# Kernel tuning notes

Hardware: AMD Instinct MI355X
Metric: run time of the kernel (lower is better)

## Reference

```python
import jax, jax.numpy as jnp
import numpy as np

NUM_HEADS = 16


def setup_inputs() -> dict:
    key = jax.random.key(0)
    ks = jax.random.split(key, 5)
    N, L, E = 4, 1024, 1024
    x = jax.random.normal(ks[0], (N, L, E), dtype=jnp.float32)
    sc = 1.0 / np.sqrt(E)
    wq = jax.random.normal(ks[1], (E, E), dtype=jnp.float32) * sc
    wk = jax.random.normal(ks[2], (E, E), dtype=jnp.float32) * sc
    wv = jax.random.normal(ks[3], (E, E), dtype=jnp.float32) * sc
    wo = jax.random.normal(ks[4], (E, E), dtype=jnp.float32) * sc
    return {"x": x, "wq": wq, "wk": wk, "wv": wv, "wo": wo}


def reference(x, wq, wk, wv, wo):
    N, L, E = x.shape
    H = NUM_HEADS
    d = E // H  # d_k = d_v = d_q
    # Linear layers: y = x @ W^T (torch Linear weight is (out, in))
    q = (x @ wq.T).reshape(N, H, L, d)  # NOTE: raw view, matches torch .view
    k = (x @ wk.T).reshape(N, H, L, d)
    v = (x @ wv.T).reshape(N, H, L, d)
    scores = jnp.einsum("nhld,nhmd->nhlm", q, k) / jnp.sqrt(jnp.float32(d))
    # causal mask (dropout is identity in eval / p=0)
    causal = jnp.tril(jnp.ones((L, L), dtype=bool))
    scores = jnp.where(causal, scores, jnp.float32(-jnp.inf))
    attn = jax.nn.softmax(scores, axis=-1)
    wei = jnp.einsum("nhlm,nhmd->nhld", attn, v).reshape(N, L, H * d)
    return wei @ wo.T
```

## Files before the change

### kernel.cpp

```cpp
#include <hip/hip_runtime.h>
#include <hip/hip_bf16.h>

using bf16 = __hip_bfloat16;
typedef __attribute__((ext_vector_type(8))) short bf16x8;
typedef __attribute__((ext_vector_type(4))) float f32x4;

#define MFMA16(a, b, c) __builtin_amdgcn_mfma_f32_16x16x32_bf16(a, b, c, 0, 0, 0)
#define SWZ(row, byteoff) ((byteoff) ^ (((row) & 7) << 4))

__device__ __forceinline__ unsigned short f2b(float f) {
  union { float f; unsigned int u; } c; c.f = f;
  unsigned int r = c.u + 0x7fffu + ((c.u >> 16) & 1u);
  return (unsigned short)(r >> 16);
}
__device__ __forceinline__ float b2f(short b) {
  union { unsigned int u; float f; } c;
  c.u = ((unsigned int)(unsigned short)b) << 16;
  return c.f;
}
__device__ __forceinline__ bf16x8 scale8(bf16x8 v, float s) {
  bf16x8 r;
#pragma unroll
  for (int j = 0; j < 8; ++j) r[j] = (short)f2b(b2f(v[j]) * s);
  return r;
}
__device__ __forceinline__ unsigned cvtpk(float a, float b) {
  unsigned r;
  asm("v_cvt_pk_bf16_f32 %0, %1, %2" : "=v"(r) : "v"(a), "v"(b));
  return r;
}

__device__ __forceinline__ void gload_lds16(const void* g, void* l) {
  __builtin_amdgcn_global_load_lds(
      (const __attribute__((address_space(1))) void*)g,
      (__attribute__((address_space(3))) void*)l, 16, 0, 0);
}

__device__ __forceinline__ void store_out(float* p, float v) { *p = v; }
__device__ __forceinline__ void store_out(bf16* p, float v) {
  *(unsigned short*)p = f2b(v);
}

__global__ __launch_bounds__(256) void cast_all(
    const float* __restrict__ x, const float* __restrict__ wq,
    const float* __restrict__ wk, const float* __restrict__ wv,
    const float* __restrict__ wo,
    unsigned short* __restrict__ xb, unsigned short* __restrict__ wqb,
    unsigned short* __restrict__ wkb, unsigned short* __restrict__ wvb,
    unsigned short* __restrict__ wob) {
  int i = blockIdx.x * 256 + threadIdx.x;
  const float* src;
  unsigned short* dst;
  int off;
  if (i < 1048576) {
    src = x; dst = xb; off = i;
  } else {
    int j = i - 1048576;
    int seg = j >> 18;
    off = j & 262143;
    src = (seg == 0) ? wq : (seg == 1) ? wk : (seg == 2) ? wv : wo;
    dst = (seg == 0) ? wqb : (seg == 1) ? wkb : (seg == 2) ? wvb : wob;
  }
  float4 v = reinterpret_cast<const float4*>(src)[off];
  ushort4 o;
  o.x = f2b(v.x); o.y = f2b(v.y); o.z = f2b(v.z); o.w = f2b(v.w);
  reinterpret_cast<ushort4*>(dst)[off] = o;
}

template <typename TOUT>
__device__ __forceinline__ void gemm_tile(const bf16* __restrict__ A,
                                          const bf16* __restrict__ Bt,
                                          TOUT* __restrict__ C, int N, int K,
                                          int bm, int bn) {
  __shared__ bf16 Asm[128 * 64];
  __shared__ bf16 Bsm[128 * 64];
  const int tid = threadIdx.x;
  const int lane = tid & 63;
  const int w = tid >> 6;
  const int wr = w >> 1, wc = w & 1;
  const int fr = lane & 15;
  const int fg = lane >> 4;
  f32x4 acc[4][4] = {};

  const int strow = w * 8 + (lane >> 3);
  const int stcb = (lane & 7) * 16;

  for (int kt = 0; kt < K; kt += 64) {
#pragma unroll
    for (int r = 0; r < 4; ++r) {
      const int row = r * 32 + strow;
      gload_lds16(
          (const char*)(A + (size_t)(bm + row) * K + kt) + SWZ(row, stcb),
          (char*)Asm + (r * 32 + w * 8) * 128);
      gload_lds16(
          (const char*)(Bt + (size_t)row * K + kt) + SWZ(row, stcb),
          (char*)Bsm + (r * 32 + w * 8) * 128);
    }
    __syncthreads();
    bf16x8 afr[4][2], bfr[4][2];
#pragma unroll
    for (int m = 0; m < 4; ++m) {
      const int row = wr * 64 + m * 16 + fr;
      const char* rp = (const char*)Asm + row * 128;
#pragma unroll
      for (int s = 0; s < 2; ++s)
        afr[m][s] = *(const bf16x8*)(rp + SWZ(row, s * 64 + fg * 16));
    }
#pragma unroll
    for (int n = 0; n < 4; ++n) {
      const int row = wc * 64 + n * 16 + fr;
      const char* rp = (const char*)Bsm + row * 128;
#pragma unroll
      for (int s = 0; s < 2; ++s)
        bfr[n][s] = *(const bf16x8*)(rp + SWZ(row, s * 64 + fg * 16));
    }
    __builtin_amdgcn_s_setprio(1);
#pragma unroll
    for (int m = 0; m < 4; ++m)
#pragma unroll
      for (int n = 0; n < 4; ++n) {
        acc[m][n] = MFMA16(afr[m][0], bfr[n][0], acc[m][n]);
        acc[m][n] = MFMA16(afr[m][1], bfr[n][1], acc[m][n]);
      }
    __builtin_amdgcn_s_setprio(0);
    __syncthreads();
  }
#pragma unroll
  for (int m = 0; m < 4; ++m) {
    const int row0 = bm + wr * 64 + m * 16 + (lane >> 4) * 4;
#pragma unroll
    for (int n = 0; n < 4; ++n) {
      const int col = bn + wc * 64 + n * 16 + fr;
#pragma unroll
      for (int r = 0; r < 4; ++r)
        store_out(&C[(size_t)(row0 + r) * N + col], acc[m][n][r]);
    }
  }
}

__global__ __launch_bounds__(256) void gemm_qkv(
    const bf16* __restrict__ A, const bf16* __restrict__ B3,
    bf16* __restrict__ Cq, bf16* __restrict__ Ck, bf16* __restrict__ Cv) {
  const int id = blockIdx.y * 32 + blockIdx.x;
  const int sw = (id & 7) * 96 + (id >> 3);
  const int bm = (sw & 31) * 128;
  const int bnG = (sw >> 5) * 128;
  bf16* C = (bnG < 1024) ? Cq : (bnG < 2048) ? Ck : Cv;
  gemm_tile<bf16>(A, B3 + (size_t)bnG * 1024, C, 1024, 1024, bm, bnG & 1023);
}

__global__ __launch_bounds__(256) void gemm_out(const bf16* __restrict__ A,
                                                const bf16* __restrict__ B,
                                                float* __restrict__ C) {
  const int id = blockIdx.y * 32 + blockIdx.x;
  const int sw = (id & 7) * 32 + (id >> 3);
  const int bm = (sw & 31) * 128;
  const int bn = (sw >> 5) * 128;
  gemm_tile<float>(A, B + (size_t)bn * 1024, C, 1024, 1024, bm, bn);
}

__global__ __launch_bounds__(256) void attn_fwd(
    const bf16* __restrict__ Q, const bf16* __restrict__ K,
    const bf16* __restrict__ V, bf16* __restrict__ O) {
  const int nh = blockIdx.x;
  const size_t base = (size_t)nh * 65536;
  const bf16* Qp = Q + base;
  const bf16* Kp = K + base;
  const bf16* Vp = V + base;
  bf16* Op = O + base;
  const int p = blockIdx.y;
  const int qiA = p, qiB = 15 - p;
  const int tid = threadIdx.x;
  const int lane = tid & 63;
  const int w = tid >> 6;
  const int fr = lane & 15;
  const int fg = lane >> 4;

  __shared__ bf16 Ksm[2][64 * 64];
  __shared__ bf16 Vts[2][64 * 64];

  const float QSC = 0.125f * 1.44269504089f;
  const float MS = 12.0f;
  const int rA0 = qiA * 64 + w * 16;
  const int rB0 = qiB * 64 + w * 16;
  bf16x8 qA[2], qB[2];
#pragma unroll
  for (int ks = 0; ks < 2; ++ks) {
    qA[ks] = scale8(
        *(const bf16x8*)&Qp[(size_t)(rA0 + fr) * 64 + ks * 32 + fg * 8], QSC);
    qB[ks] = scale8(
        *(const bf16x8*)&Qp[(size_t)(rB0 + fr) * 64 + ks * 32 + fg * 8], QSC);
  }

  float sA = 0.f, sB = 0.f;
  f32x4 oA[4], oB[4];
#pragma unroll
  for (int d = 0; d < 4; ++d) {
    oA[d] = (f32x4){0.f, 0.f, 0.f, 0.f};
    oB[d] = (f32x4){0.f, 0.f, 0.f, 0.f};
  }

  const int NKV = qiB + 1;
  const int qloc = w * 16 + fr;

  const int bkv = (tid & 15) * 4;
  const int bd = (tid >> 4) * 4;
  union VU { ushort4 v; unsigned short s[4]; };
  VU v4[4], nv4[4];

  const int krow = w * 16 + (lane >> 3);
  const int kcb = (lane & 7) * 16;

#define STAGE_K(kt, bi)                                                       \
  {                                                                           \
    _Pragma("unroll") for (int i = 0; i < 2; ++i) {                           \
      const int row = krow + i * 8;                                           \
      gload_lds16((const char*)Kp + ((size_t)((kt)*64 + row) * 128 +          \
                                     SWZ(row, kcb)),                          \
                  (char*)&Ksm[bi][0] + (w * 16 + i * 8) * 128);               \
    }                                                                         \
  }
#define LOAD_V(kt, r)                                                         \
  {                                                                           \
    _Pragma("unroll") for (int j = 0; j < 4; ++j) (r)[j].v =                  \
        *(const ushort4*)(Vp + (size_t)((kt)*64 + bkv + j) * 64 + bd);        \
  }
#define WRITE_V(bi, r)                                                        \
  {                                                                           \
    _Pragma("unroll") for (int i = 0; i < 4; ++i) {                           \
      VU o4;                                                                  \
      _Pragma("unroll") for (int j = 0; j < 4; ++j) o4.s[j] = (r)[j].s[i];    \
      const int row = bd + i;                                                 \
      *(ushort4*)((char*)&Vts[bi][0] + row * 128 + SWZ(row, bkv * 2)) = o4.v; \
    }                                                                         \
  }

  STAGE_K(0, 0);
  LOAD_V(0, v4);
  WRITE_V(0, v4);
  __syncthreads();

  union PU { bf16x8 v; unsigned u[4]; };
  union VF { bf16x8 v; unsigned long long q[2]; };

  for (int kt = 0; kt < NKV; ++kt) {
    const int b = kt & 1;
    const bool more = (kt + 1 < NKV);
    if (more) {
      STAGE_K(kt + 1, b ^ 1);
      LOAD_V(kt + 1, nv4);
    }
    const bool aAct = (kt <= qiA);

    bf16x8 kf[4][2];
#pragma unroll
    for (int c = 0; c < 4; ++c) {
      const int row = c * 16 + fr;
      const char* rp = (const char*)&Ksm[b][0] + row * 128;
      kf[c][0] = *(const bf16x8*)(rp + SWZ(row, fg * 16));
      kf[c][1] = *(const bf16x8*)(rp + SWZ(row, 64 + fg * 16));
    }
    VF vf[4][2];
#pragma unroll
    for (int d = 0; d < 4; ++d) {
      const int row = d * 16 + fr;
      const char* rp = (const char*)&Vts[b][0] + row * 128;
#pragma unroll
      for (int ks = 0; ks < 2; ++ks) {
        vf[d][ks].q[0] =
            *(const unsigned long long*)(rp + SWZ(row, ks * 64 + fg * 8));
        vf[d][ks].q[1] =
            *(const unsigned long long*)(rp + SWZ(row, ks * 64 + 32 + fg * 8));
      }
    }

    auto strip_sm = [&](const bf16x8 (&qf)[2], float& s, bool diag,
                        PU (&pa)[2]) {
      f32x4 sc[4];
      __builtin_amdgcn_s_setprio(1);
#pragma unroll
      for (int c = 0; c < 4; ++c) {
        f32x4 acc = (f32x4){0.f, 0.f, 0.f, 0.f};
        acc = MFMA16(kf[c][0], qf[0], acc);
        acc = MFMA16(kf[c][1], qf[1], acc);
        sc[c] = acc;
      }
      __builtin_amdgcn_s_setprio(0);
      float pv[4][4];
#pragma unroll
      for (int c = 0; c < 4; ++c)
#pragma unroll
        for (int r = 0; r < 4; ++r) {
          float sv = sc[c][r];
          if (diag) {
            const int kvloc = c * 16 + fg * 4 + r;
            sv = (kvloc <= qloc) ? sv : -INFINITY;
          }
          const float e = __builtin_amdgcn_exp2f(sv - MS);
          pv[c][r] = e;
          s += e;
        }
#pragma unroll
      for (int ks = 0; ks < 2; ++ks) {
        pa[ks].u[0] = cvtpk(pv[ks * 2][0], pv[ks * 2][1]);
        pa[ks].u[1] = cvtpk(pv[ks * 2][2], pv[ks * 2][3]);
        pa[ks].u[2] = cvtpk(pv[ks * 2 + 1][0], pv[ks * 2 + 1][1]);
        pa[ks].u[3] = cvtpk(pv[ks * 2 + 1][2], pv[ks * 2 + 1][3]);
      }
    };

    PU paA[2], paB[2];
    strip_sm(qB, sB, kt == qiB, paB);
    if (aAct) strip_sm(qA, sA, kt == qiA, paA);

    __builtin_amdgcn_s_setprio(1);
#pragma unroll
    for (int d = 0; d < 4; ++d) {
      oB[d] = MFMA16(paB[0].v, vf[d][0].v, oB[d]);
      oB[d] = MFMA16(paB[1].v, vf[d][1].v, oB[d]);
    }
    if (aAct) {
#pragma unroll
      for (int d = 0; d < 4; ++d) {
        oA[d] = MFMA16(paA[0].v, vf[d][0].v, oA[d]);
        oA[d] = MFMA16(paA[1].v, vf[d][1].v, oA[d]);
      }
    }
    __builtin_amdgcn_s_setprio(0);

    if (more) WRITE_V(b ^ 1, nv4);
    __syncthreads();
  }

  sA += __shfl_xor(sA, 16); sA += __shfl_xor(sA, 32);
  sB += __shfl_xor(sB, 16); sB += __shfl_xor(sB, 32);
  float sAo[4], sBo[4];
#pragma unroll
  for (int r = 0; r < 4; ++r) {
    sAo[r] = __shfl(sA, fg * 4 + r);
    sBo[r] = __shfl(sB, fg * 4 + r);
  }

#pragma unroll
  for (int d = 0; d < 4; ++d)
#pragma unroll
    for (int r = 0; r < 4; ++r) {
      const float vA = oA[d][r] / sAo[r];
      const float vB = oB[d][r] / sBo[r];
      *(unsigned short*)&Op[(size_t)(rA0 + fg * 4 + r) * 64 + d * 16 + fr] =
          f2b(vA);
      *(unsigned short*)&Op[(size_t)(rB0 + fg * 4 + r) * 64 + d * 16 + fr] =
          f2b(vB);
    }
#undef STAGE_K
#undef LOAD_V
#undef WRITE_V
}

extern "C" void kernel_launch(void* const* d_in, const int* in_sizes, int n_in,
                              void* d_out, int out_size, void* d_ws,
                              size_t ws_size, hipStream_t stream) {
  const float* x = (const float*)d_in[0];
  const float* wq = (const float*)d_in[1];
  const float* wk = (const float*)d_in[2];
  const float* wv = (const float*)d_in[3];
  const float* wo = (const float*)d_in[4];
  float* out = (float*)d_out;
  char* ws = (char*)d_ws;

  bf16* xb = (bf16*)(ws);
  bf16* wqkv = (bf16*)(ws + (8u << 20));
  bf16* wqb = wqkv;
  bf16* wkb = (bf16*)(ws + (10u << 20));
  bf16* wvb = (bf16*)(ws + (12u << 20));
  bf16* wob = (bf16*)(ws + (14u << 20));
  bf16* qbuf = (bf16*)(ws + (16u << 20));
  bf16* kbuf = (bf16*)(ws + (24u << 20));
  bf16* vbuf = (bf16*)(ws + (32u << 20));
  bf16* weib = (bf16*)(ws);

  cast_all<<<8192, 256, 0, stream>>>(x, wq, wk, wv, wo, (unsigned short*)xb,
                                     (unsigned short*)wqb, (unsigned short*)wkb,
                                     (unsigned short*)wvb, (unsigned short*)wob);
  gemm_qkv<<<dim3(32, 24), 256, 0, stream>>>(xb, wqkv, qbuf, kbuf, vbuf);
  attn_fwd<<<dim3(64, 8), 256, 0, stream>>>(qbuf, kbuf, vbuf, weib);
  gemm_out<<<dim3(32, 8), 256, 0, stream>>>(weib, wob, out);
}
```

Measured before the change: 94.45 us.

## Split attention KV loop across two blocks and combine partial outputs

Doubles the attention grid by having each block process only every other KV tile (even or odd phase), writing unnormalized partial outputs and row sums to workspace. A new combine kernel adds the two partials and divides by the summed denominators. The split is meant to raise occupancy on a 256-CU device, where the original 512-block grid underfills it. It relies on the fixed max-shift softmax so partials can simply be added, and it costs an extra kernel launch, extra global traffic, and bf16 rounding of the unnormalized partials.

```diff
diff --git a/kernel.cpp b/kernel.cpp
--- a/kernel.cpp
+++ b/kernel.cpp
@@ -159,16 +159,19 @@
   gemm_tile<float>(A, B + (size_t)bn * 1024, C, 1024, 1024, bm, bn);
 }
 
-__global__ __launch_bounds__(256) void attn_fwd(
+template <int SPLIT>
+__global__ __launch_bounds__(256) void attn_fwd_t(
     const bf16* __restrict__ Q, const bf16* __restrict__ K,
-    const bf16* __restrict__ V, bf16* __restrict__ O) {
+    const bf16* __restrict__ V, bf16* __restrict__ O,
+    bf16* __restrict__ P1, float* __restrict__ S0, float* __restrict__ S1) {
   const int nh = blockIdx.x;
   const size_t base = (size_t)nh * 65536;
   const bf16* Qp = Q + base;
   const bf16* Kp = K + base;
   const bf16* Vp = V + base;
-  bf16* Op = O + base;
   const int p = blockIdx.y;
+  const int phase = SPLIT ? blockIdx.z : 0;
+  const int step = SPLIT ? 2 : 1;
   const int qiA = p, qiB = 15 - p;
   const int tid = threadIdx.x;
   const int lane = tid & 63;
@@ -235,20 +238,21 @@
     }                                                                         \
   }
 
-  STAGE_K(0, 0);
-  LOAD_V(0, v4);
+  STAGE_K(phase, 0);
+  LOAD_V(phase, v4);
   WRITE_V(0, v4);
   __syncthreads();
 
   union PU { bf16x8 v; unsigned u[4]; };
   union VF { bf16x8 v; unsigned long long q[2]; };
 
-  for (int kt = 0; kt < NKV; ++kt) {
-    const int b = kt & 1;
-    const bool more = (kt + 1 < NKV);
+  int it = 0;
+  for (int kt = phase; kt < NKV; kt += step, ++it) {
+    const int b = it & 1;
+    const bool more = (kt + step < NKV);
     if (more) {
-      STAGE_K(kt + 1, b ^ 1);
-      LOAD_V(kt + 1, nv4);
+      STAGE_K(kt + step, b ^ 1);
+      LOAD_V(kt + step, nv4);
     }
     const bool aAct = (kt <= qiA);
 
@@ -334,27 +338,62 @@
 
   sA += __shfl_xor(sA, 16); sA += __shfl_xor(sA, 32);
   sB += __shfl_xor(sB, 16); sB += __shfl_xor(sB, 32);
-  float sAo[4], sBo[4];
-#pragma unroll
-  for (int r = 0; r < 4; ++r) {
-    sAo[r] = __shfl(sA, fg * 4 + r);
-    sBo[r] = __shfl(sB, fg * 4 + r);
-  }
-
-#pragma unroll
-  for (int d = 0; d < 4; ++d)
+
+  if (SPLIT) {
+    bf16* OPp = ((phase == 0) ? O : P1) + base;
+    float* SP = (phase == 0) ? S0 : S1;
+    if (fg == 0) {
+      SP[(size_t)nh * 1024 + rA0 + fr] = sA;
+      SP[(size_t)nh * 1024 + rB0 + fr] = sB;
+    }
+#pragma unroll
+    for (int d = 0; d < 4; ++d)
+#pragma unroll
+      for (int r = 0; r < 4; ++r) {
+        *(unsigned short*)&OPp[(size_t)(rA0 + fg * 4 + r) * 64 + d * 16 + fr] =
+            f2b(oA[d][r]);
+        *(unsigned short*)&OPp[(size_t)(rB0 + fg * 4 + r) * 64 + d * 16 + fr] =
+            f2b(oB[d][r]);
+      }
+  } else {
+    bf16* Op = O + base;
+    float sAo[4], sBo[4];
 #pragma unroll
     for (int r = 0; r < 4; ++r) {
-      const float vA = oA[d][r] / sAo[r];
-      const float vB = oB[d][r] / sBo[r];
-      *(unsigned short*)&Op[(size_t)(rA0 + fg * 4 + r) * 64 + d * 16 + fr] =
-          f2b(vA);
-      *(unsigned short*)&Op[(size_t)(rB0 + fg * 4 + r) * 64 + d * 16 + fr] =
-          f2b(vB);
-    }
+      sAo[r] = __shfl(sA, fg * 4 + r);
+      sBo[r] = __shfl(sB, fg * 4 + r);
+    }
+#pragma unroll
+    for (int d = 0; d < 4; ++d)
+#pragma unroll
+      for (int r = 0; r < 4; ++r) {
+        const float vA = oA[d][r] / sAo[r];
+        const float vB = oB[d][r] / sBo[r];
+        *(unsigned short*)&Op[(size_t)(rA0 + fg * 4 + r) * 64 + d * 16 + fr] =
+            f2b(vA);
+        *(unsigned short*)&Op[(size_t)(rB0 + fg * 4 + r) * 64 + d * 16 + fr] =
+            f2b(vB);
+      }
+  }
 #undef STAGE_K
 #undef LOAD_V
 #undef WRITE_V
+}
+
+__global__ __launch_bounds__(256) void attn_combine(
+    bf16* __restrict__ P0, const bf16* __restrict__ P1,
+    const float* __restrict__ S0, const float* __restrict__ S1) {
+  const int i4 = blockIdx.x * 256 + threadIdx.x;
+  const int q = i4 >> 4;
+  ushort4 a = reinterpret_cast<const ushort4*>(P0)[i4];
+  ushort4 b = reinterpret_cast<const ushort4*>(P1)[i4];
+  const float inv = 1.0f / (S0[q] + S1[q]);
+  ushort4 o;
+  o.x = f2b((b2f((short)a.x) + b2f((short)b.x)) * inv);
+  o.y = f2b((b2f((short)a.y) + b2f((short)b.y)) * inv);
+  o.z = f2b((b2f((short)a.z) + b2f((short)b.z)) * inv);
+  o.w = f2b((b2f((short)a.w) + b2f((short)b.w)) * inv);
+  reinterpret_cast<ushort4*>(P0)[i4] = o;
 }
 
 extern "C" void kernel_launch(void* const* d_in, const int* in_sizes, int n_in,
@@ -378,11 +417,22 @@
   bf16* kbuf = (bf16*)(ws + (24u << 20));
   bf16* vbuf = (bf16*)(ws + (32u << 20));
   bf16* weib = (bf16*)(ws);
+  bf16* part1 = (bf16*)(ws + (40u << 20));
+  float* s0 = (float*)(ws + (48u << 20));
+  float* s1 = (float*)(ws + (48u << 20) + (256u << 10));
+  const bool use_split = ws_size >= ((48u << 20) + (512u << 10));
 
   cast_all<<<8192, 256, 0, stream>>>(x, wq, wk, wv, wo, (unsigned short*)xb,
                                      (unsigned short*)wqb, (unsigned short*)wkb,
                                      (unsigned short*)wvb, (unsigned short*)wob);
   gemm_qkv<<<dim3(32, 24), 256, 0, stream>>>(xb, wqkv, qbuf, kbuf, vbuf);
-  attn_fwd<<<dim3(64, 8), 256, 0, stream>>>(qbuf, kbuf, vbuf, weib);
+  if (use_split) {
+    attn_fwd_t<1><<<dim3(64, 8, 2), 256, 0, stream>>>(qbuf, kbuf, vbuf, weib,
+                                                      part1, s0, s1);
+    attn_combine<<<4096, 256, 0, stream>>>(weib, part1, s0, s1);
+  } else {
+    attn_fwd_t<0><<<dim3(64, 8), 256, 0, stream>>>(qbuf, kbuf, vbuf, weib,
+                                                   nullptr, nullptr, nullptr);
+  }
   gemm_out<<<dim3(32, 8), 256, 0, stream>>>(weib, wob, out);
 }
```

After: 101.0 us. +6.9%, slower.

## Process two KV tiles per sync in attention; use 128x64 tiles for output GEMM

Applied to the files above, without the earlier changes.

The attention kernel now stages and computes two 64-row KV tiles per loop iteration, using four K/V LDS buffers. This halves the number of __syncthreads barriers and issues twice as many loads ahead of compute. The output projection replaces the shared 128x128 tile GEMM with a dedicated 128x64 tile kernel, giving 512 blocks instead of 256 to fill the GPU better. The cost is doubled LDS use in attention, which may reduce occupancy. The new GEMM uses a single buffer with no prefetch, so loads are not overlapped with compute.

```diff
diff --git a/kernel.cpp b/kernel.cpp
--- a/kernel.cpp
+++ b/kernel.cpp
@@ -149,14 +149,83 @@
   gemm_tile<bf16>(A, B3 + (size_t)bnG * 1024, C, 1024, 1024, bm, bnG & 1023);
 }
 
-__global__ __launch_bounds__(256) void gemm_out(const bf16* __restrict__ A,
-                                                const bf16* __restrict__ B,
-                                                float* __restrict__ C) {
+__global__ __launch_bounds__(256) void gemm_out64(const bf16* __restrict__ A,
+                                                  const bf16* __restrict__ B,
+                                                  float* __restrict__ C) {
+  __shared__ bf16 Asm[128 * 64];
+  __shared__ bf16 Bsm[64 * 64];
   const int id = blockIdx.y * 32 + blockIdx.x;
-  const int sw = (id & 7) * 32 + (id >> 3);
+  const int sw = (id & 7) * 64 + (id >> 3);
   const int bm = (sw & 31) * 128;
-  const int bn = (sw >> 5) * 128;
-  gemm_tile<float>(A, B + (size_t)bn * 1024, C, 1024, 1024, bm, bn);
+  const int bn = (sw >> 5) * 64;
+  const bf16* Bt = B + (size_t)bn * 1024;
+
+  const int tid = threadIdx.x;
+  const int lane = tid & 63;
+  const int w = tid >> 6;
+  const int wr = w >> 1, wc = w & 1;
+  const int fr = lane & 15;
+  const int fg = lane >> 4;
+  f32x4 acc[4][2] = {};
+
+  const int strow = w * 8 + (lane >> 3);
+  const int stcb = (lane & 7) * 16;
+
+  for (int kt = 0; kt < 1024; kt += 64) {
+#pragma unroll
+    for (int r = 0; r < 4; ++r) {
+      const int row = r * 32 + strow;
+      gload_lds16(
+          (const char*)(A + (size_t)(bm + row) * 1024 + kt) + SWZ(row, stcb),
+          (char*)Asm + (r * 32 + w * 8) * 128);
+    }
+#pragma unroll
+    for (int r = 0; r < 2; ++r) {
+      const int row = r * 32 + strow;
+      gload_lds16(
+          (const char*)(Bt + (size_t)row * 1024 + kt) + SWZ(row, stcb),
+          (char*)Bsm + (r * 32 + w * 8) * 128);
+    }
+    __syncthreads();
+    bf16x8 afr[4][2], bfr[2][2];
+#pragma unroll
+    for (int m = 0; m < 4; ++m) {
+      const int row = wr * 64 + m * 16 + fr;
+      const char* rp = (const char*)Asm + row * 128;
+#pragma unroll
+      for (int s = 0; s < 2; ++s)
+        afr[m][s] = *(const bf16x8*)(rp + SWZ(row, s * 64 + fg * 16));
+    }
+#pragma unroll
+    for (int n = 0; n < 2; ++n) {
+      const int row = wc * 32 + n * 16 + fr;
+      const char* rp = (const char*)Bsm + row * 128;
+#pragma unroll
+      for (int s = 0; s < 2; ++s)
+        bfr[n][s] = *(const bf16x8*)(rp + SWZ(row, s * 64 + fg * 16));
+    }
+    __builtin_amdgcn_s_setprio(1);
+#pragma unroll
+    for (int m = 0; m < 4; ++m)
+#pragma unroll
+      for (int n = 0; n < 2; ++n) {
+        acc[m][n] = MFMA16(afr[m][0], bfr[n][0], acc[m][n]);
+        acc[m][n] = MFMA16(afr[m][1], bfr[n][1], acc[m][n]);
+      }
+    __builtin_amdgcn_s_setprio(0);
+    __syncthreads();
+  }
+#pragma unroll
+  for (int m = 0; m < 4; ++m) {
+    const int row0 = bm + wr * 64 + m * 16 + fg * 4;
+#pragma unroll
+    for (int n = 0; n < 2; ++n) {
+      const int col = bn + wc * 32 + n * 16 + fr;
+#pragma unroll
+      for (int r = 0; r < 4; ++r)
+        C[(size_t)(row0 + r) * 1024 + col] = acc[m][n][r];
+    }
+  }
 }
 
 __global__ __launch_bounds__(256) void attn_fwd(
@@ -176,8 +245,8 @@
   const int fr = lane & 15;
   const int fg = lane >> 4;
 
-  __shared__ bf16 Ksm[2][64 * 64];
-  __shared__ bf16 Vts[2][64 * 64];
+  __shared__ bf16 Ksm[2][2][64 * 64];
+  __shared__ bf16 Vts[2][2][64 * 64];
 
   const float QSC = 0.125f * 1.44269504089f;
   const float MS = 12.0f;
@@ -206,18 +275,18 @@
   const int bkv = (tid & 15) * 4;
   const int bd = (tid >> 4) * 4;
   union VU { ushort4 v; unsigned short s[4]; };
-  VU v4[4], nv4[4];
+  VU v4a[4], v4b[4];
 
   const int krow = w * 16 + (lane >> 3);
   const int kcb = (lane & 7) * 16;
 
-#define STAGE_K(kt, bi)                                                       \
+#define STAGE_K(kt, dst)                                                      \
   {                                                                           \
     _Pragma("unroll") for (int i = 0; i < 2; ++i) {                           \
       const int row = krow + i * 8;                                           \
       gload_lds16((const char*)Kp + ((size_t)((kt)*64 + row) * 128 +          \
                                      SWZ(row, kcb)),                          \
-                  (char*)&Ksm[bi][0] + (w * 16 + i * 8) * 128);               \
+                  (char*)(dst) + (w * 16 + i * 8) * 128);                     \
     }                                                                         \
   }
 #define LOAD_V(kt, r)                                                         \
@@ -225,38 +294,26 @@
     _Pragma("unroll") for (int j = 0; j < 4; ++j) (r)[j].v =                  \
         *(const ushort4*)(Vp + (size_t)((kt)*64 + bkv + j) * 64 + bd);        \
   }
-#define WRITE_V(bi, r)                                                        \
+#define WRITE_V(dst, r)                                                       \
   {                                                                           \
     _Pragma("unroll") for (int i = 0; i < 4; ++i) {                           \
       VU o4;                                                                  \
       _Pragma("unroll") for (int j = 0; j < 4; ++j) o4.s[j] = (r)[j].s[i];    \
       const int row = bd + i;                                                 \
-      *(ushort4*)((char*)&Vts[bi][0] + row * 128 + SWZ(row, bkv * 2)) = o4.v; \
+      *(ushort4*)((char*)(dst) + row * 128 + SWZ(row, bkv * 2)) = o4.v;       \
     }                                                                         \
   }
-
-  STAGE_K(0, 0);
-  LOAD_V(0, v4);
-  WRITE_V(0, v4);
-  __syncthreads();
 
   union PU { bf16x8 v; unsigned u[4]; };
   union VF { bf16x8 v; unsigned long long q[2]; };
 
-  for (int kt = 0; kt < NKV; ++kt) {
-    const int b = kt & 1;
-    const bool more = (kt + 1 < NKV);
-    if (more) {
-      STAGE_K(kt + 1, b ^ 1);
-      LOAD_V(kt + 1, nv4);
-    }
+  auto compute_tile = [&](int kt, const char* kb, const char* vb) {
     const bool aAct = (kt <= qiA);
-
     bf16x8 kf[4][2];
 #pragma unroll
     for (int c = 0; c < 4; ++c) {
       const int row = c * 16 + fr;
-      const char* rp = (const char*)&Ksm[b][0] + row * 128;
+      const char* rp = kb + row * 128;
       kf[c][0] = *(const bf16x8*)(rp + SWZ(row, fg * 16));
       kf[c][1] = *(const bf16x8*)(rp + SWZ(row, 64 + fg * 16));
     }
@@ -264,7 +321,7 @@
 #pragma unroll
     for (int d = 0; d < 4; ++d) {
       const int row = d * 16 + fr;
-      const char* rp = (const char*)&Vts[b][0] + row * 128;
+      const char* rp = vb + row * 128;
 #pragma unroll
       for (int ks = 0; ks < 2; ++ks) {
         vf[d][ks].q[0] =
@@ -327,8 +384,38 @@
       }
     }
     __builtin_amdgcn_s_setprio(0);
-
-    if (more) WRITE_V(b ^ 1, nv4);
+  };
+
+  STAGE_K(0, &Ksm[0][0][0]);
+  STAGE_K(1, &Ksm[0][1][0]);
+  LOAD_V(0, v4a);
+  LOAD_V(1, v4b);
+  WRITE_V(&Vts[0][0][0], v4a);
+  WRITE_V(&Vts[0][1][0], v4b);
+  __syncthreads();
+
+  const int I = (NKV + 1) >> 1;
+  for (int it = 0; it < I; ++it) {
+    const int kt0 = 2 * it;
+    const int b = it & 1;
+    const bool more0 = (kt0 + 2 < NKV);
+    const bool more1 = (kt0 + 3 < NKV);
+    if (more0) {
+      STAGE_K(kt0 + 2, &Ksm[b ^ 1][0][0]);
+      LOAD_V(kt0 + 2, v4a);
+    }
+    if (more1) {
+      STAGE_K(kt0 + 3, &Ksm[b ^ 1][1][0]);
+      LOAD_V(kt0 + 3, v4b);
+    }
+
+    compute_tile(kt0, (const char*)&Ksm[b][0][0], (const char*)&Vts[b][0][0]);
+    if (kt0 + 1 < NKV)
+      compute_tile(kt0 + 1, (const char*)&Ksm[b][1][0],
+                   (const char*)&Vts[b][1][0]);
+
+    if (more0) WRITE_V(&Vts[b ^ 1][0][0], v4a);
+    if (more1) WRITE_V(&Vts[b ^ 1][1][0], v4b);
     __syncthreads();
   }
 
@@ -384,5 +471,5 @@
                                      (unsigned short*)wvb, (unsigned short*)wob);
   gemm_qkv<<<dim3(32, 24), 256, 0, stream>>>(xb, wqkv, qbuf, kbuf, vbuf);
   attn_fwd<<<dim3(64, 8), 256, 0, stream>>>(qbuf, kbuf, vbuf, weib);
-  gemm_out<<<dim3(32, 8), 256, 0, stream>>>(weib, wob, out);
-}
+  gemm_out64<<<dim3(32, 16), 256, 0, stream>>>(weib, wob, out);
+}
```

After: 86.74 us. 1.09x faster.
